# Kernel tuning notes

Measured on AMD Instinct MI355X. Metric: run time of the kernel, lower is better.

The kernel has to match this reference:

```python
import jax, jax.numpy as jnp
import numpy as np

N_HEADS = 8
D_EMBED = 512
D_HEAD = D_EMBED // N_HEADS


def setup_inputs() -> dict:
    key = jax.random.key(0)
    ks = jax.random.split(key, 5)
    x = jax.random.normal(ks[0], (1, 4096, D_EMBED), dtype=jnp.float32)
    # in_proj: Linear(d, 3d); out_proj: Linear(d, d). Stored as [in, out] for x @ W.
    scale_in = 1.0 / np.sqrt(D_EMBED)
    W_in = jax.random.uniform(ks[1], (D_EMBED, 3 * D_EMBED), jnp.float32, -scale_in, scale_in)
    b_in = jax.random.uniform(ks[2], (3 * D_EMBED,), jnp.float32, -scale_in, scale_in)
    W_out = jax.random.uniform(ks[3], (D_EMBED, D_EMBED), jnp.float32, -scale_in, scale_in)
    b_out = jax.random.uniform(ks[4], (D_EMBED,), jnp.float32, -scale_in, scale_in)
    return {"x": x, "W_in": W_in, "b_in": b_in, "W_out": W_out, "b_out": b_out,
            "causal_mask": 1}


def reference(x, W_in, b_in, W_out, b_out, causal_mask):
    B, S, D = x.shape
    qkv = x @ W_in + b_in                      # [B, S, 3D]
    q, k, v = jnp.split(qkv, 3, axis=-1)
    # [B, S, D] -> [B, H, S, d_head]
    def split_heads(t):
        return t.reshape(B, S, N_HEADS, D_HEAD).transpose(0, 2, 1, 3)
    q, k, v = split_heads(q), split_heads(k), split_heads(v)
    weight = jnp.einsum("bhqd,bhkd->bhqk", q, k)  # [B, H, S, S]
    if causal_mask:
        mask = jnp.triu(jnp.ones((S, S), dtype=bool), k=1)
        weight = jnp.where(mask, -jnp.inf, weight)
    weight = weight / jnp.sqrt(jnp.float32(D_HEAD)).astype(weight.dtype)
    weight = jax.nn.softmax(weight, axis=-1)
    out = jnp.einsum("bhqk,bhkd->bhqd", weight, v)  # [B, H, S, d_head]
    out = out.transpose(0, 2, 1, 3).reshape(B, S, D)
    return out @ W_out + b_out
```

## Files before the change

### kernel.cpp

```cpp
#include <hip/hip_runtime.h>
#include <math.h>

#define SEQ 4096
#define DM 512
#define NH 8
#define DH 64
#define TQK (3 * DM)
#define QSCALE 0.18033688011112042f

typedef __attribute__((ext_vector_type(8))) short bf16x8;
typedef __attribute__((ext_vector_type(4))) float floatx4;
typedef unsigned short ushort_t;

__device__ __forceinline__ floatx4 mfma16(bf16x8 a, bf16x8 b, floatx4 c) {
    return __builtin_amdgcn_mfma_f32_16x16x32_bf16(a, b, c, 0, 0, 0);
}
__device__ __forceinline__ float ex2(float x) { return __builtin_amdgcn_exp2f(x); }

__device__ __forceinline__ unsigned int pk2(float a, float b) {
    unsigned int ua = __float_as_uint(a); ua = (ua + 0x7FFFu + ((ua >> 16) & 1u)) >> 16;
    unsigned int ub = __float_as_uint(b); ub = (ub + 0x7FFFu + ((ub >> 16) & 1u)) >> 16;
    return ua | (ub << 16);
}
__device__ __forceinline__ unsigned short f2bf(float x) {
    unsigned int u = __float_as_uint(x);
    return (unsigned short)((u + 0x7FFFu + ((u >> 16) & 1u)) >> 16);
}
__device__ __forceinline__ float bflo(unsigned int u) { return __uint_as_float(u << 16); }
__device__ __forceinline__ float bfhi(unsigned int u) { return __uint_as_float(u & 0xFFFF0000u); }

__device__ __forceinline__ void gload_lds16(const void* g, void* l) {
    __builtin_amdgcn_global_load_lds(
        (const __attribute__((address_space(1))) unsigned int*)g,
        (__attribute__((address_space(3))) unsigned int*)l, 16, 0, 0);
}

#define DPPMAX(x, ctrl) \
    (x) = fmaxf((x), __int_as_float(__builtin_amdgcn_update_dpp(0, __float_as_int(x), (ctrl), 0xF, 0xF, true)))
__device__ __forceinline__ float row_max16(float x) {
    DPPMAX(x, 0xB1);
    DPPMAX(x, 0x4E);
    DPPMAX(x, 0x141);
    DPPMAX(x, 0x140);
    return x;
}

__global__ __launch_bounds__(256) void prep(const float* __restrict__ x,
                                            const float* __restrict__ W_in,
                                            const float* __restrict__ W_out,
                                            ushort_t* __restrict__ xb,
                                            ushort_t* __restrict__ wti,
                                            ushort_t* __restrict__ wto) {
    __shared__ float T[64][65];
    const int bid = blockIdx.x, tid = threadIdx.x;
    if (bid < 1024) {
        const int i = bid * 256 + tid;
        const float4* p = (const float4*)x + (size_t)i * 2;
        float4 f0 = p[0], f1 = p[1];
        ((uint4*)xb)[i] = make_uint4(pk2(f0.x, f0.y), pk2(f0.z, f0.w),
                                     pk2(f1.x, f1.y), pk2(f1.z, f1.w));
        return;
    }
    const float* W; ushort_t* WT; int N, K, n0, k0; bool qscale;
    if (bid < 1216) { int id = bid - 1024; W = W_in;  WT = wti; N = TQK; K = DM;
                      n0 = (id % 24) * 64; k0 = (id / 24) * 64; qscale = true; }
    else            { int id = bid - 1216; W = W_out; WT = wto; N = DM;  K = DM;
                      n0 = (id % 8) * 64;  k0 = (id / 8) * 64;  qscale = false; }
    {
        const int r = tid >> 2, g = tid & 3;
        const float* src = W + (size_t)(k0 + r) * N + n0 + g * 16;
#pragma unroll
        for (int i = 0; i < 4; i++) {
            float4 f = ((const float4*)src)[i];
            T[g * 16 + i * 4 + 0][r] = f.x;
            T[g * 16 + i * 4 + 1][r] = f.y;
            T[g * 16 + i * 4 + 2][r] = f.z;
            T[g * 16 + i * 4 + 3][r] = f.w;
        }
    }
    __syncthreads();
    const int nr = tid >> 2, g2 = tid & 3;
    const float sc = (qscale && (n0 + nr < DM)) ? QSCALE : 1.0f;
    unsigned int pk[8];
#pragma unroll
    for (int j = 0; j < 8; j++)
        pk[j] = pk2(T[nr][g2 * 16 + 2 * j] * sc, T[nr][g2 * 16 + 2 * j + 1] * sc);
    ushort_t* dst = WT + (size_t)(n0 + nr) * K + k0 + g2 * 16;
    ((uint4*)dst)[0] = make_uint4(pk[0], pk[1], pk[2], pk[3]);
    ((uint4*)dst)[1] = make_uint4(pk[4], pk[5], pk[6], pk[7]);
}

__global__ __launch_bounds__(256) void gemm_in(const ushort_t* __restrict__ A,
                                               const ushort_t* __restrict__ BT,
                                               const float* __restrict__ bias,
                                               ushort_t* __restrict__ Cv,
                                               ushort_t* __restrict__ vt_out) {
    __shared__ __align__(16) ushort_t As[2][128 * 64];
    __shared__ __align__(16) ushort_t Bs[2][128 * 64];
    const int tid  = threadIdx.x;
    const int lane = tid & 63;
    const int w    = tid >> 6;
    const int quad = lane >> 4;
    const int ln   = lane & 15;
    const int row0 = blockIdx.y * 128;
    const int col0 = blockIdx.x * 128;
    const int wm = w >> 1, wn = w & 1;
    const int srow = lane >> 3;
    const int js   = (lane & 7) ^ srow;
    const int K = DM, N = TQK;

    floatx4 acc[4][4];
#pragma unroll
    for (int i = 0; i < 4; i++)
#pragma unroll
        for (int j = 0; j < 4; j++) acc[i][j] = (floatx4){0.f, 0.f, 0.f, 0.f};

#pragma unroll
    for (int i = 0; i < 4; i++) {
        const int c = w * 4 + i;
        gload_lds16(A  + (size_t)(row0 + c * 8 + srow) * K + js * 8, &As[0][c * 512]);
        gload_lds16(BT + (size_t)(col0 + c * 8 + srow) * K + js * 8, &Bs[0][c * 512]);
    }

    for (int kt = 0; kt < 8; kt++) {
        const int cur = kt & 1;
        __syncthreads();
        if (kt < 7) {
            const int k0n = (kt + 1) << 6;
#pragma unroll
            for (int i = 0; i < 4; i++) {
                const int c = w * 4 + i;
                gload_lds16(A  + (size_t)(row0 + c * 8 + srow) * K + k0n + js * 8, &As[cur ^ 1][c * 512]);
                gload_lds16(BT + (size_t)(col0 + c * 8 + srow) * K + k0n + js * 8, &Bs[cur ^ 1][c * 512]);
            }
        }
#pragma unroll
        for (int s = 0; s < 2; s++) {
            bf16x8 af[4], bfr[4];
#pragma unroll
            for (int i = 0; i < 4; i++) {
                const int lm = wm * 64 + i * 16 + ln;
                af[i] = *(const bf16x8*)&As[cur][lm * 64 + ((s * 4 + quad) ^ (ln & 7)) * 8];
                const int lnn = wn * 64 + i * 16 + ln;
                bfr[i] = *(const bf16x8*)&Bs[cur][lnn * 64 + ((s * 4 + quad) ^ (ln & 7)) * 8];
            }
#pragma unroll
            for (int i = 0; i < 4; i++)
#pragma unroll
                for (int j = 0; j < 4; j++)
                    acc[i][j] = mfma16(af[i], bfr[j], acc[i][j]);
        }
    }

    if (col0 >= 2 * DM) {
#pragma unroll
        for (int j = 0; j < 4; j++) {
            const int n = col0 + wn * 64 + j * 16 + ln;
            const float bv = bias[n];
#pragma unroll
            for (int i = 0; i < 4; i++) {
                const int mb = row0 + wm * 64 + i * 16 + quad * 4;
                uint2 pkd;
                pkd.x = pk2(acc[i][j][0] + bv, acc[i][j][1] + bv);
                pkd.y = pk2(acc[i][j][2] + bv, acc[i][j][3] + bv);
                *(uint2*)&vt_out[(size_t)(n - 2 * DM) * SEQ + mb] = pkd;
            }
        }
        return;
    }

#pragma unroll
    for (int j = 0; j < 4; j++) {
        const int n = col0 + wn * 64 + j * 16 + ln;
        const float bv = bias[n] * ((n < DM) ? QSCALE : 1.0f);
#pragma unroll
        for (int i = 0; i < 4; i++) {
            const int mb = row0 + wm * 64 + i * 16 + quad * 4;
#pragma unroll
            for (int r = 0; r < 4; r++)
                Cv[(size_t)(mb + r) * N + n] = f2bf(acc[i][j][r] + bv);
        }
    }
}

__global__ __launch_bounds__(512) void attn_split(const ushort_t* __restrict__ qkv_b,
                                                  const ushort_t* __restrict__ vt,
                                                  ushort_t* __restrict__ po,
                                                  float2* __restrict__ pml) {
    __shared__ __align__(16) ushort_t Ks[2][64 * 64];
    __shared__ __align__(16) ushort_t Vs[2][64 * 64];
    __shared__ __align__(16) ushort_t Ps[128 * 72];

    const int tid  = threadIdx.x;
    const int lane = tid & 63;
    const int w    = tid >> 6;
    const int quad = lane >> 4;
    const int ln   = lane & 15;
    const int h    = blockIdx.y;

    const int e = 143 - (int)blockIdx.x;
    int g = 0;
    while (e >= 2 * (g + 1) * (g + 2)) g++;
    const int off = e - 2 * g * (g + 1);
    const int nc  = g + 1;
    const int qt  = 4 * g + off / nc;
    const int c   = off % nc;
    const int T   = 2 * qt + 2;
    const int jt0 = (c * T) / nc;
    const int jt1 = ((c + 1) * T) / nc;
    const int q0  = qt * 128;

    const ushort_t* qrow = qkv_b + (size_t)(q0 + w * 16 + ln) * TQK + h * DH;
    const bf16x8 a0 = *(const bf16x8*)(qrow + quad * 8);
    const bf16x8 a1 = *(const bf16x8*)(qrow + quad * 8 + 32);

    const short oneb = (short)0x3F80;
    const bf16x8 vone = {oneb, oneb, oneb, oneb, oneb, oneb, oneb, oneb};

    float m_q = -INFINITY;
    floatx4 o[4], ol;
#pragma unroll
    for (int t = 0; t < 4; t++) o[t] = (floatx4){0.f, 0.f, 0.f, 0.f};
    ol = (floatx4){0.f, 0.f, 0.f, 0.f};

    const int srow = lane >> 3;
    const int js   = (lane & 7) ^ srow;

    {
        const int k0 = jt0 * 64;
        gload_lds16(qkv_b + (size_t)(k0 + w * 8 + srow) * TQK + DM + h * DH + js * 8,
                    &Ks[0][w * 512]);
        gload_lds16(vt + (size_t)(h * DH + w * 8 + srow) * SEQ + k0 + js * 8,
                    &Vs[0][w * 512]);
    }

    for (int jt = jt0; jt < jt1; ++jt) {
        const int cur = (jt - jt0) & 1;
        const int k0  = jt * 64;
        __syncthreads();
        if (jt + 1 < jt1) {
            const int k0n = (jt + 1) * 64;
            gload_lds16(qkv_b + (size_t)(k0n + w * 8 + srow) * TQK + DM + h * DH + js * 8,
                        &Ks[cur ^ 1][w * 512]);
            gload_lds16(vt + (size_t)(h * DH + w * 8 + srow) * SEQ + k0n + js * 8,
                        &Vs[cur ^ 1][w * 512]);
        }

        floatx4 sa[4];
#pragma unroll
        for (int t = 0; t < 4; t++) {
            const int n = t * 16 + ln;
            const bf16x8 b0 = *(const bf16x8*)&Ks[cur][n * 64 + ((quad) ^ (ln & 7)) * 8];
            const bf16x8 b1 = *(const bf16x8*)&Ks[cur][n * 64 + ((4 + quad) ^ (ln & 7)) * 8];
            floatx4 acc = {0.f, 0.f, 0.f, 0.f};
            acc = mfma16(a0, b0, acc);
            acc = mfma16(a1, b1, acc);
            sa[t] = acc;
        }

        if (k0 + 63 > q0 + w * 16) {
#pragma unroll
            for (int t = 0; t < 4; t++) {
                const int cg2 = k0 + t * 16 + ln;
#pragma unroll
                for (int r = 0; r < 4; r++) {
                    const int rg = q0 + w * 16 + quad * 4 + r;
                    if (cg2 > rg) sa[t][r] = -INFINITY;
                }
            }
        }

        float mx = sa[0][0];
#pragma unroll
        for (int t = 0; t < 4; t++)
#pragma unroll
            for (int r = 0; r < 4; r++) mx = fmaxf(mx, sa[t][r]);
        mx = row_max16(mx);
        const float mn = fmaxf(fmaxf(m_q, mx), -1e30f);
        const float alpha = ex2(m_q - mn);
        m_q = mn;
#pragma unroll
        for (int t = 0; t < 4; t++)
#pragma unroll
            for (int r = 0; r < 4; r++) {
                const float p = ex2(sa[t][r] - mn);
                Ps[(w * 16 + quad * 4 + r) * 72 + t * 16 + ln] =
                    (ushort_t)(__float_as_uint(p) >> 16);
            }
        if (alpha < 1.0f) {
#pragma unroll
            for (int t = 0; t < 4; t++)
#pragma unroll
                for (int r = 0; r < 4; r++) o[t][r] *= alpha;
#pragma unroll
            for (int r = 0; r < 4; r++) ol[r] *= alpha;
        }

        __builtin_amdgcn_wave_barrier();

        const bf16x8 p0 = *(const bf16x8*)&Ps[(w * 16 + ln) * 72 + quad * 8];
        const bf16x8 p1 = *(const bf16x8*)&Ps[(w * 16 + ln) * 72 + quad * 8 + 32];
#pragma unroll
        for (int t = 0; t < 4; t++) {
            const int d = t * 16 + ln;
            const bf16x8 v0 = *(const bf16x8*)&Vs[cur][d * 64 + ((quad) ^ (ln & 7)) * 8];
            const bf16x8 v1 = *(const bf16x8*)&Vs[cur][d * 64 + ((4 + quad) ^ (ln & 7)) * 8];
            o[t] = mfma16(p0, v0, o[t]);
            o[t] = mfma16(p1, v1, o[t]);
        }
        ol = mfma16(p0, vone, ol);
        ol = mfma16(p1, vone, ol);
    }

    const size_t pbase  = ((size_t)h * 144 + e) * (128 * 64);
    const size_t mlbase = ((size_t)h * 144 + e) * 128;
#pragma unroll
    for (int t = 0; t < 4; t++)
#pragma unroll
        for (int r = 0; r < 4; r++)
            po[pbase + (size_t)(w * 16 + quad * 4 + r) * 64 + t * 16 + ln] = f2bf(o[t][r]);
    if (ln == 0) {
#pragma unroll
        for (int r = 0; r < 4; r++)
            pml[mlbase + w * 16 + quad * 4 + r] = make_float2(m_q, ol[r]);
    }
}

__global__ __launch_bounds__(512) void attn_combine(const ushort_t* __restrict__ po,
                                                    const float2* __restrict__ pml,
                                                    ushort_t* __restrict__ aob) {
    const int qt = blockIdx.x, h = blockIdx.y;
    const int gq = qt >> 2;
    const int nc = gq + 1;
    const int sbase = 2 * gq * (gq + 1) + (qt & 3) * nc;
    const int row = threadIdx.x >> 2, g = threadIdx.x & 3;

    float2 ml[8];
    float M = -INFINITY;
    for (int ci = 0; ci < nc; ci++) {
        ml[ci] = pml[((size_t)h * 144 + sbase + ci) * 128 + row];
        M = fmaxf(M, ml[ci].x);
    }
    float L = 0.f;
    float acc[16];
#pragma unroll
    for (int j = 0; j < 16; j++) acc[j] = 0.f;

    for (int ci = 0; ci < nc; ci++) {
        const float wgt = ex2(ml[ci].x - M);
        L += wgt * ml[ci].y;
        const ushort_t* p = po + ((size_t)h * 144 + sbase + ci) * (128 * 64)
                               + (size_t)row * 64 + g * 16;
        uint4 u0 = ((const uint4*)p)[0];
        uint4 u1 = ((const uint4*)p)[1];
        const unsigned int uu[8] = {u0.x, u0.y, u0.z, u0.w, u1.x, u1.y, u1.z, u1.w};
#pragma unroll
        for (int j = 0; j < 8; j++) {
            acc[2 * j]     += wgt * bflo(uu[j]);
            acc[2 * j + 1] += wgt * bfhi(uu[j]);
        }
    }
    const float inv = 1.0f / L;
    unsigned int pk[8];
#pragma unroll
    for (int j = 0; j < 8; j++)
        pk[j] = pk2(acc[2 * j] * inv, acc[2 * j + 1] * inv);
    ushort_t* dst = aob + (size_t)(qt * 128 + row) * DM + h * DH + g * 16;
    ((uint4*)dst)[0] = make_uint4(pk[0], pk[1], pk[2], pk[3]);
    ((uint4*)dst)[1] = make_uint4(pk[4], pk[5], pk[6], pk[7]);
}

__global__ __launch_bounds__(256) void gemm_out(const ushort_t* __restrict__ A,
                                                const ushort_t* __restrict__ BT,
                                                const float* __restrict__ bias,
                                                float* __restrict__ out) {
    __shared__ __align__(16) ushort_t As[2][128 * 64];
    __shared__ __align__(16) ushort_t Bs[2][64 * 64];
    const int tid  = threadIdx.x;
    const int lane = tid & 63;
    const int w    = tid >> 6;
    const int quad = lane >> 4;
    const int ln   = lane & 15;
    const int row0 = blockIdx.y * 128;
    const int col0 = blockIdx.x * 64;
    const int wm = w >> 1, wn = w & 1;
    const int srow = lane >> 3;
    const int js   = (lane & 7) ^ srow;

    floatx4 acc[4][2];
#pragma unroll
    for (int i = 0; i < 4; i++)
#pragma unroll
        for (int j = 0; j < 2; j++) acc[i][j] = (floatx4){0.f, 0.f, 0.f, 0.f};

#pragma unroll
    for (int i = 0; i < 4; i++) {
        const int c = w * 4 + i;
        gload_lds16(A + (size_t)(row0 + c * 8 + srow) * DM + js * 8, &As[0][c * 512]);
    }
#pragma unroll
    for (int i = 0; i < 2; i++) {
        const int c = w * 2 + i;
        gload_lds16(BT + (size_t)(col0 + c * 8 + srow) * DM + js * 8, &Bs[0][c * 512]);
    }

    for (int kt = 0; kt < 8; kt++) {
        const int cur = kt & 1;
        __syncthreads();
        if (kt < 7) {
            const int k0n = (kt + 1) << 6;
#pragma unroll
            for (int i = 0; i < 4; i++) {
                const int c = w * 4 + i;
                gload_lds16(A + (size_t)(row0 + c * 8 + srow) * DM + k0n + js * 8, &As[cur ^ 1][c * 512]);
            }
#pragma unroll
            for (int i = 0; i < 2; i++) {
                const int c = w * 2 + i;
                gload_lds16(BT + (size_t)(col0 + c * 8 + srow) * DM + k0n + js * 8, &Bs[cur ^ 1][c * 512]);
            }
        }
#pragma unroll
        for (int s = 0; s < 2; s++) {
            bf16x8 af[4], bfr[2];
#pragma unroll
            for (int i = 0; i < 4; i++) {
                const int lm = wm * 64 + i * 16 + ln;
                af[i] = *(const bf16x8*)&As[cur][lm * 64 + ((s * 4 + quad) ^ (ln & 7)) * 8];
            }
#pragma unroll
            for (int j = 0; j < 2; j++) {
                const int lnn = wn * 32 + j * 16 + ln;
                bfr[j] = *(const bf16x8*)&Bs[cur][lnn * 64 + ((s * 4 + quad) ^ (ln & 7)) * 8];
            }
#pragma unroll
            for (int i = 0; i < 4; i++)
#pragma unroll
                for (int j = 0; j < 2; j++)
                    acc[i][j] = mfma16(af[i], bfr[j], acc[i][j]);
        }
    }

#pragma unroll
    for (int j = 0; j < 2; j++) {
        const int n = col0 + wn * 32 + j * 16 + ln;
        const float bv = bias[n];
#pragma unroll
        for (int i = 0; i < 4; i++) {
            const int mb = row0 + wm * 64 + i * 16 + quad * 4;
#pragma unroll
            for (int r = 0; r < 4; r++)
                out[(size_t)(mb + r) * DM + n] = acc[i][j][r] + bv;
        }
    }
}

extern "C" void kernel_launch(void* const* d_in, const int* in_sizes, int n_in,
                              void* d_out, int out_size, void* d_ws, size_t ws_size,
                              hipStream_t stream) {
    const float* x     = (const float*)d_in[0];
    const float* W_in  = (const float*)d_in[1];
    const float* b_in  = (const float*)d_in[2];
    const float* W_out = (const float*)d_in[3];
    const float* b_out = (const float*)d_in[4];
    float* out = (float*)d_out;

    char* ws = (char*)d_ws;
    ushort_t* xb    = (ushort_t*)ws;
    ushort_t* wti   = (ushort_t*)(ws + (4u  << 20));
    ushort_t* wto   = (ushort_t*)(ws + (6u  << 20));
    ushort_t* qkv_b = (ushort_t*)(ws + (7u  << 20));
    ushort_t* vtb   = (ushort_t*)(ws + (19u << 20));
    ushort_t* po    = (ushort_t*)(ws + (23u << 20));
    float2*   pml   = (float2*)  (ws + (42u << 20));
    ushort_t* aob   = (ushort_t*)(ws + (44u << 20));

    prep<<<1280, 256, 0, stream>>>(x, W_in, W_out, xb, wti, wto);

    gemm_in<<<dim3(TQK / 128, SEQ / 128), 256, 0, stream>>>(xb, wti, b_in, qkv_b, vtb);

    attn_split<<<dim3(144, NH), 512, 0, stream>>>(qkv_b, vtb, po, pml);

    attn_combine<<<dim3(SEQ / 128, NH), 512, 0, stream>>>(po, pml, aob);

    gemm_out<<<dim3(DM / 64, SEQ / 128), 256, 0, stream>>>(aob, wto, b_out, out);
}
```

Measured before the change: 156.0 us.

## Restructure attention split kernel to keep P in registers with transposed S

The attention split kernel now computes S transposed (K as A operand), so each lane's exp'd probabilities can be packed straight into bf16 operands for a 16x16x16 MFMA against V. This removes the P round-trip through shared memory and the extra ones-vector MFMAs that tracked the row sum, which is now accumulated with cross-lane shuffles instead. Blocks shrink to 256 threads, with each wave handling two 16-row query groups so loaded K/V fragments are reused twice, and the work-tile ordering is recomputed with a loop. The trade-offs are more register pressure, truncating rather than rounding P and the output to bf16, and a split ordering that must stay consistent with the combine kernel.

```diff
diff --git a/kernel.cpp b/kernel.cpp
--- a/kernel.cpp
+++ b/kernel.cpp
@@ -9,11 +9,15 @@
 #define QSCALE 0.18033688011112042f
 
 typedef __attribute__((ext_vector_type(8))) short bf16x8;
+typedef __attribute__((ext_vector_type(4))) short short4v;
 typedef __attribute__((ext_vector_type(4))) float floatx4;
 typedef unsigned short ushort_t;
 
 __device__ __forceinline__ floatx4 mfma16(bf16x8 a, bf16x8 b, floatx4 c) {
     return __builtin_amdgcn_mfma_f32_16x16x32_bf16(a, b, c, 0, 0, 0);
+}
+__device__ __forceinline__ floatx4 mfma16k16(short4v a, short4v b, floatx4 c) {
+    return __builtin_amdgcn_mfma_f32_16x16x16bf16_1k(a, b, c, 0, 0, 0);
 }
 __device__ __forceinline__ float ex2(float x) { return __builtin_amdgcn_exp2f(x); }
 
@@ -26,23 +30,19 @@
     unsigned int u = __float_as_uint(x);
     return (unsigned short)((u + 0x7FFFu + ((u >> 16) & 1u)) >> 16);
 }
+__device__ __forceinline__ unsigned int pkt(float a, float b) {
+    return __builtin_amdgcn_perm(__float_as_uint(b), __float_as_uint(a), 0x07060302u);
+}
 __device__ __forceinline__ float bflo(unsigned int u) { return __uint_as_float(u << 16); }
 __device__ __forceinline__ float bfhi(unsigned int u) { return __uint_as_float(u & 0xFFFF0000u); }
+__device__ __forceinline__ short4v mk4(unsigned int lo, unsigned int hi) {
+    union { unsigned int u[2]; short4v v; } x; x.u[0] = lo; x.u[1] = hi; return x.v;
+}
 
 __device__ __forceinline__ void gload_lds16(const void* g, void* l) {
     __builtin_amdgcn_global_load_lds(
         (const __attribute__((address_space(1))) unsigned int*)g,
         (__attribute__((address_space(3))) unsigned int*)l, 16, 0, 0);
-}
-
-#define DPPMAX(x, ctrl) \
-    (x) = fmaxf((x), __int_as_float(__builtin_amdgcn_update_dpp(0, __float_as_int(x), (ctrl), 0xF, 0xF, true)))
-__device__ __forceinline__ float row_max16(float x) {
-    DPPMAX(x, 0xB1);
-    DPPMAX(x, 0x4E);
-    DPPMAX(x, 0x141);
-    DPPMAX(x, 0x140);
-    return x;
 }
 
 __global__ __launch_bounds__(256) void prep(const float* __restrict__ x,
@@ -183,13 +183,12 @@
     }
 }
 
-__global__ __launch_bounds__(512) void attn_split(const ushort_t* __restrict__ qkv_b,
-                                                  const ushort_t* __restrict__ vt,
-                                                  ushort_t* __restrict__ po,
-                                                  float2* __restrict__ pml) {
+__global__ __launch_bounds__(256, 3) void attn_split(const ushort_t* __restrict__ qkv_b,
+                                                     const ushort_t* __restrict__ vt,
+                                                     ushort_t* __restrict__ po,
+                                                     float2* __restrict__ pml) {
     __shared__ __align__(16) ushort_t Ks[2][64 * 64];
     __shared__ __align__(16) ushort_t Vs[2][64 * 64];
-    __shared__ __align__(16) ushort_t Ps[128 * 72];
 
     const int tid  = threadIdx.x;
     const int lane = tid & 63;
@@ -197,41 +196,51 @@
     const int quad = lane >> 4;
     const int ln   = lane & 15;
     const int h    = blockIdx.y;
-
-    const int e = 143 - (int)blockIdx.x;
-    int g = 0;
-    while (e >= 2 * (g + 1) * (g + 2)) g++;
-    const int off = e - 2 * g * (g + 1);
-    const int nc  = g + 1;
-    const int qt  = 4 * g + off / nc;
-    const int c   = off % nc;
+    const int lnx7 = ln & 7;
+    const int qh   = quad >> 1, ql = quad & 1;
+
+    int qt = 0, nc = 1, cc = 0;
+    {
+        int bx = blockIdx.x, acc = 0;
+        for (int q = 31; q >= 0; --q) {
+            const int n = (q >> 2) + 1;
+            if (bx < acc + n) { qt = q; nc = n; cc = bx - acc; break; }
+            acc += n;
+        }
+    }
     const int T   = 2 * qt + 2;
-    const int jt0 = (c * T) / nc;
-    const int jt1 = ((c + 1) * T) / nc;
+    const int jt0 = (cc * T) / nc;
+    const int jt1 = ((cc + 1) * T) / nc;
     const int q0  = qt * 128;
 
-    const ushort_t* qrow = qkv_b + (size_t)(q0 + w * 16 + ln) * TQK + h * DH;
-    const bf16x8 a0 = *(const bf16x8*)(qrow + quad * 8);
-    const bf16x8 a1 = *(const bf16x8*)(qrow + quad * 8 + 32);
-
-    const short oneb = (short)0x3F80;
-    const bf16x8 vone = {oneb, oneb, oneb, oneb, oneb, oneb, oneb, oneb};
-
-    float m_q = -INFINITY;
-    floatx4 o[4], ol;
-#pragma unroll
-    for (int t = 0; t < 4; t++) o[t] = (floatx4){0.f, 0.f, 0.f, 0.f};
-    ol = (floatx4){0.f, 0.f, 0.f, 0.f};
+    bf16x8 qb[2][2];
+#pragma unroll
+    for (int qg = 0; qg < 2; qg++) {
+        const ushort_t* qr = qkv_b + (size_t)(q0 + w * 32 + qg * 16 + ln) * TQK + h * DH;
+        qb[qg][0] = *(const bf16x8*)(qr + quad * 8);
+        qb[qg][1] = *(const bf16x8*)(qr + quad * 8 + 32);
+    }
+
+    float m_[2] = {-INFINITY, -INFINITY}, l_[2] = {0.f, 0.f};
+    floatx4 o[2][4];
+#pragma unroll
+    for (int qg = 0; qg < 2; qg++)
+#pragma unroll
+        for (int dt = 0; dt < 4; dt++) o[qg][dt] = (floatx4){0.f, 0.f, 0.f, 0.f};
 
     const int srow = lane >> 3;
     const int js   = (lane & 7) ^ srow;
 
     {
         const int k0 = jt0 * 64;
-        gload_lds16(qkv_b + (size_t)(k0 + w * 8 + srow) * TQK + DM + h * DH + js * 8,
-                    &Ks[0][w * 512]);
-        gload_lds16(vt + (size_t)(h * DH + w * 8 + srow) * SEQ + k0 + js * 8,
-                    &Vs[0][w * 512]);
+#pragma unroll
+        for (int i = 0; i < 2; i++) {
+            const int cg = w * 2 + i;
+            gload_lds16(qkv_b + (size_t)(k0 + cg * 8 + srow) * TQK + DM + h * DH + js * 8,
+                        &Ks[0][cg * 512]);
+            gload_lds16(vt + (size_t)(h * DH + cg * 8 + srow) * SEQ + k0 + js * 8,
+                        &Vs[0][cg * 512]);
+        }
     }
 
     for (int jt = jt0; jt < jt1; ++jt) {
@@ -240,89 +249,111 @@
         __syncthreads();
         if (jt + 1 < jt1) {
             const int k0n = (jt + 1) * 64;
-            gload_lds16(qkv_b + (size_t)(k0n + w * 8 + srow) * TQK + DM + h * DH + js * 8,
-                        &Ks[cur ^ 1][w * 512]);
-            gload_lds16(vt + (size_t)(h * DH + w * 8 + srow) * SEQ + k0n + js * 8,
-                        &Vs[cur ^ 1][w * 512]);
-        }
-
-        floatx4 sa[4];
+#pragma unroll
+            for (int i = 0; i < 2; i++) {
+                const int cg = w * 2 + i;
+                gload_lds16(qkv_b + (size_t)(k0n + cg * 8 + srow) * TQK + DM + h * DH + js * 8,
+                            &Ks[cur ^ 1][cg * 512]);
+                gload_lds16(vt + (size_t)(h * DH + cg * 8 + srow) * SEQ + k0n + js * 8,
+                            &Vs[cur ^ 1][cg * 512]);
+            }
+        }
+
+        bf16x8 kf[4][2];
 #pragma unroll
         for (int t = 0; t < 4; t++) {
-            const int n = t * 16 + ln;
-            const bf16x8 b0 = *(const bf16x8*)&Ks[cur][n * 64 + ((quad) ^ (ln & 7)) * 8];
-            const bf16x8 b1 = *(const bf16x8*)&Ks[cur][n * 64 + ((4 + quad) ^ (ln & 7)) * 8];
-            floatx4 acc = {0.f, 0.f, 0.f, 0.f};
-            acc = mfma16(a0, b0, acc);
-            acc = mfma16(a1, b1, acc);
-            sa[t] = acc;
-        }
-
-        if (k0 + 63 > q0 + w * 16) {
+            kf[t][0] = *(const bf16x8*)&Ks[cur][(t * 16 + ln) * 64 + ((quad) ^ lnx7) * 8];
+            kf[t][1] = *(const bf16x8*)&Ks[cur][(t * 16 + ln) * 64 + ((4 + quad) ^ lnx7) * 8];
+        }
+        short4v vf[4][4];
+#pragma unroll
+        for (int t = 0; t < 4; t++)
+#pragma unroll
+            for (int dt = 0; dt < 4; dt++)
+                vf[t][dt] = *(const short4v*)&Vs[cur][(dt * 16 + ln) * 64 +
+                                                     (((2 * t + qh) ^ lnx7) << 3) + (ql << 2)];
+
+#pragma unroll
+        for (int qg = 0; qg < 2; qg++) {
+            const int q = q0 + w * 32 + qg * 16 + ln;
+
+            floatx4 sa[4];
 #pragma unroll
             for (int t = 0; t < 4; t++) {
-                const int cg2 = k0 + t * 16 + ln;
+                floatx4 a = (floatx4){0.f, 0.f, 0.f, 0.f};
+                a = mfma16(kf[t][0], qb[qg][0], a);
+                a = mfma16(kf[t][1], qb[qg][1], a);
+                sa[t] = a;
+            }
+
+            if (k0 + 63 > q0 + w * 32 + qg * 16) {
+#pragma unroll
+                for (int t = 0; t < 4; t++)
+#pragma unroll
+                    for (int r = 0; r < 4; r++) {
+                        const int key = k0 + t * 16 + quad * 4 + r;
+                        if (key > q) sa[t][r] = -INFINITY;
+                    }
+            }
+
+            float mx = sa[0][0];
+#pragma unroll
+            for (int t = 0; t < 4; t++)
+#pragma unroll
+                for (int r = 0; r < 4; r++) mx = fmaxf(mx, sa[t][r]);
+            mx = fmaxf(mx, __shfl_xor(mx, 16));
+            mx = fmaxf(mx, __shfl_xor(mx, 32));
+            const float mn = fmaxf(fmaxf(m_[qg], mx), -1e30f);
+            const float alpha = ex2(m_[qg] - mn);
+            m_[qg] = mn;
+
+            float p[4][4];
+            float ls = 0.f;
+#pragma unroll
+            for (int t = 0; t < 4; t++)
 #pragma unroll
                 for (int r = 0; r < 4; r++) {
-                    const int rg = q0 + w * 16 + quad * 4 + r;
-                    if (cg2 > rg) sa[t][r] = -INFINITY;
+                    p[t][r] = ex2(sa[t][r] - mn);
+                    ls += p[t][r];
                 }
-            }
-        }
-
-        float mx = sa[0][0];
-#pragma unroll
-        for (int t = 0; t < 4; t++)
-#pragma unroll
-            for (int r = 0; r < 4; r++) mx = fmaxf(mx, sa[t][r]);
-        mx = row_max16(mx);
-        const float mn = fmaxf(fmaxf(m_q, mx), -1e30f);
-        const float alpha = ex2(m_q - mn);
-        m_q = mn;
-#pragma unroll
-        for (int t = 0; t < 4; t++)
-#pragma unroll
-            for (int r = 0; r < 4; r++) {
-                const float p = ex2(sa[t][r] - mn);
-                Ps[(w * 16 + quad * 4 + r) * 72 + t * 16 + ln] =
-                    (ushort_t)(__float_as_uint(p) >> 16);
-            }
-        if (alpha < 1.0f) {
+            ls += __shfl_xor(ls, 16);
+            ls += __shfl_xor(ls, 32);
+            l_[qg] = l_[qg] * alpha + ls;
+
+            float a4[4];
+#pragma unroll
+            for (int r = 0; r < 4; r++)
+                a4[r] = __shfl(alpha, (lane & 48) | (quad * 4 + r));
+#pragma unroll
+            for (int dt = 0; dt < 4; dt++)
+#pragma unroll
+                for (int r = 0; r < 4; r++) o[qg][dt][r] *= a4[r];
+
+            short4v pf[4];
 #pragma unroll
             for (int t = 0; t < 4; t++)
-#pragma unroll
-                for (int r = 0; r < 4; r++) o[t][r] *= alpha;
-#pragma unroll
-            for (int r = 0; r < 4; r++) ol[r] *= alpha;
-        }
-
-        __builtin_amdgcn_wave_barrier();
-
-        const bf16x8 p0 = *(const bf16x8*)&Ps[(w * 16 + ln) * 72 + quad * 8];
-        const bf16x8 p1 = *(const bf16x8*)&Ps[(w * 16 + ln) * 72 + quad * 8 + 32];
-#pragma unroll
-        for (int t = 0; t < 4; t++) {
-            const int d = t * 16 + ln;
-            const bf16x8 v0 = *(const bf16x8*)&Vs[cur][d * 64 + ((quad) ^ (ln & 7)) * 8];
-            const bf16x8 v1 = *(const bf16x8*)&Vs[cur][d * 64 + ((4 + quad) ^ (ln & 7)) * 8];
-            o[t] = mfma16(p0, v0, o[t]);
-            o[t] = mfma16(p1, v1, o[t]);
-        }
-        ol = mfma16(p0, vone, ol);
-        ol = mfma16(p1, vone, ol);
-    }
-
-    const size_t pbase  = ((size_t)h * 144 + e) * (128 * 64);
-    const size_t mlbase = ((size_t)h * 144 + e) * 128;
-#pragma unroll
-    for (int t = 0; t < 4; t++)
-#pragma unroll
-        for (int r = 0; r < 4; r++)
-            po[pbase + (size_t)(w * 16 + quad * 4 + r) * 64 + t * 16 + ln] = f2bf(o[t][r]);
-    if (ln == 0) {
-#pragma unroll
-        for (int r = 0; r < 4; r++)
-            pml[mlbase + w * 16 + quad * 4 + r] = make_float2(m_q, ol[r]);
+                pf[t] = mk4(pkt(p[t][0], p[t][1]), pkt(p[t][2], p[t][3]));
+
+#pragma unroll
+            for (int dt = 0; dt < 4; dt++)
+#pragma unroll
+                for (int t = 0; t < 4; t++)
+                    o[qg][dt] = mfma16k16(pf[t], vf[t][dt], o[qg][dt]);
+        }
+    }
+
+    const size_t pbase  = ((size_t)h * 144 + blockIdx.x) * (128 * 64);
+    const size_t mlbase = ((size_t)h * 144 + blockIdx.x) * 128;
+#pragma unroll
+    for (int qg = 0; qg < 2; qg++) {
+#pragma unroll
+        for (int dt = 0; dt < 4; dt++)
+#pragma unroll
+            for (int r = 0; r < 4; r++)
+                po[pbase + (size_t)(w * 32 + qg * 16 + quad * 4 + r) * 64 + dt * 16 + ln] =
+                    (ushort_t)(__float_as_uint(o[qg][dt][r]) >> 16);
+        if (quad == 0)
+            pml[mlbase + w * 32 + qg * 16 + ln] = make_float2(m_[qg], l_[qg]);
     }
 }
 
@@ -330,9 +361,9 @@
                                                     const float2* __restrict__ pml,
                                                     ushort_t* __restrict__ aob) {
     const int qt = blockIdx.x, h = blockIdx.y;
-    const int gq = qt >> 2;
-    const int nc = gq + 1;
-    const int sbase = 2 * gq * (gq + 1) + (qt & 3) * nc;
+    const int nc = (qt >> 2) + 1;
+    int sbase = 0;
+    for (int q = 31; q > qt; --q) sbase += (q >> 2) + 1;
     const int row = threadIdx.x >> 2, g = threadIdx.x & 3;
 
     float2 ml[8];
@@ -479,7 +510,7 @@
 
     gemm_in<<<dim3(TQK / 128, SEQ / 128), 256, 0, stream>>>(xb, wti, b_in, qkv_b, vtb);
 
-    attn_split<<<dim3(144, NH), 512, 0, stream>>>(qkv_b, vtb, po, pml);
+    attn_split<<<dim3(144, NH), 256, 0, stream>>>(qkv_b, vtb, po, pml);
 
     attn_combine<<<dim3(SEQ / 128, NH), 512, 0, stream>>>(po, pml, aob);
 
```

Measured after the change: 192.8 us. +23.6%, slower.

## Process two query row groups per wave in attention split kernel

Applied to the files above, without the earlier changes.

The attention split kernel now runs 4 waves of 256 threads instead of 8, and each wave handles 32 query rows as two 16-row groups. K fragments are loaded from LDS once and reused for both groups, and V fragments are likewise shared across the two P·V products. This halves LDS fragment reads per MFMA and the block synchronization cost. In exchange each wave holds more registers, and with launch bounds (256,3) there are fewer waves in flight to hide latency.

```diff
diff --git a/kernel.cpp b/kernel.cpp
--- a/kernel.cpp
+++ b/kernel.cpp
@@ -183,10 +183,10 @@
     }
 }
 
-__global__ __launch_bounds__(512) void attn_split(const ushort_t* __restrict__ qkv_b,
-                                                  const ushort_t* __restrict__ vt,
-                                                  ushort_t* __restrict__ po,
-                                                  float2* __restrict__ pml) {
+__global__ __launch_bounds__(256, 3) void attn_split(const ushort_t* __restrict__ qkv_b,
+                                                     const ushort_t* __restrict__ vt,
+                                                     ushort_t* __restrict__ po,
+                                                     float2* __restrict__ pml) {
     __shared__ __align__(16) ushort_t Ks[2][64 * 64];
     __shared__ __align__(16) ushort_t Vs[2][64 * 64];
     __shared__ __align__(16) ushort_t Ps[128 * 72];
@@ -197,6 +197,7 @@
     const int quad = lane >> 4;
     const int ln   = lane & 15;
     const int h    = blockIdx.y;
+    const int lnx7 = ln & 7;
 
     const int e = 143 - (int)blockIdx.x;
     int g = 0;
@@ -210,28 +211,39 @@
     const int jt1 = ((c + 1) * T) / nc;
     const int q0  = qt * 128;
 
-    const ushort_t* qrow = qkv_b + (size_t)(q0 + w * 16 + ln) * TQK + h * DH;
-    const bf16x8 a0 = *(const bf16x8*)(qrow + quad * 8);
-    const bf16x8 a1 = *(const bf16x8*)(qrow + quad * 8 + 32);
+    bf16x8 a0[2], a1[2];
+#pragma unroll
+    for (int qg = 0; qg < 2; qg++) {
+        const ushort_t* qrow = qkv_b + (size_t)(q0 + w * 32 + qg * 16 + ln) * TQK + h * DH;
+        a0[qg] = *(const bf16x8*)(qrow + quad * 8);
+        a1[qg] = *(const bf16x8*)(qrow + quad * 8 + 32);
+    }
 
     const short oneb = (short)0x3F80;
     const bf16x8 vone = {oneb, oneb, oneb, oneb, oneb, oneb, oneb, oneb};
 
-    float m_q = -INFINITY;
-    floatx4 o[4], ol;
-#pragma unroll
-    for (int t = 0; t < 4; t++) o[t] = (floatx4){0.f, 0.f, 0.f, 0.f};
-    ol = (floatx4){0.f, 0.f, 0.f, 0.f};
+    float m_q[2] = {-INFINITY, -INFINITY};
+    floatx4 o[2][4], ol[2];
+#pragma unroll
+    for (int qg = 0; qg < 2; qg++) {
+#pragma unroll
+        for (int t = 0; t < 4; t++) o[qg][t] = (floatx4){0.f, 0.f, 0.f, 0.f};
+        ol[qg] = (floatx4){0.f, 0.f, 0.f, 0.f};
+    }
 
     const int srow = lane >> 3;
     const int js   = (lane & 7) ^ srow;
 
     {
         const int k0 = jt0 * 64;
-        gload_lds16(qkv_b + (size_t)(k0 + w * 8 + srow) * TQK + DM + h * DH + js * 8,
-                    &Ks[0][w * 512]);
-        gload_lds16(vt + (size_t)(h * DH + w * 8 + srow) * SEQ + k0 + js * 8,
-                    &Vs[0][w * 512]);
+#pragma unroll
+        for (int i = 0; i < 2; i++) {
+            const int cg = w * 2 + i;
+            gload_lds16(qkv_b + (size_t)(k0 + cg * 8 + srow) * TQK + DM + h * DH + js * 8,
+                        &Ks[0][cg * 512]);
+            gload_lds16(vt + (size_t)(h * DH + cg * 8 + srow) * SEQ + k0 + js * 8,
+                        &Vs[0][cg * 512]);
+        }
     }
 
     for (int jt = jt0; jt < jt1; ++jt) {
@@ -240,89 +252,110 @@
         __syncthreads();
         if (jt + 1 < jt1) {
             const int k0n = (jt + 1) * 64;
-            gload_lds16(qkv_b + (size_t)(k0n + w * 8 + srow) * TQK + DM + h * DH + js * 8,
-                        &Ks[cur ^ 1][w * 512]);
-            gload_lds16(vt + (size_t)(h * DH + w * 8 + srow) * SEQ + k0n + js * 8,
-                        &Vs[cur ^ 1][w * 512]);
-        }
-
-        floatx4 sa[4];
+#pragma unroll
+            for (int i = 0; i < 2; i++) {
+                const int cg = w * 2 + i;
+                gload_lds16(qkv_b + (size_t)(k0n + cg * 8 + srow) * TQK + DM + h * DH + js * 8,
+                            &Ks[cur ^ 1][cg * 512]);
+                gload_lds16(vt + (size_t)(h * DH + cg * 8 + srow) * SEQ + k0n + js * 8,
+                            &Vs[cur ^ 1][cg * 512]);
+            }
+        }
+
+        bf16x8 kb0[4], kb1[4];
 #pragma unroll
         for (int t = 0; t < 4; t++) {
             const int n = t * 16 + ln;
-            const bf16x8 b0 = *(const bf16x8*)&Ks[cur][n * 64 + ((quad) ^ (ln & 7)) * 8];
-            const bf16x8 b1 = *(const bf16x8*)&Ks[cur][n * 64 + ((4 + quad) ^ (ln & 7)) * 8];
-            floatx4 acc = {0.f, 0.f, 0.f, 0.f};
-            acc = mfma16(a0, b0, acc);
-            acc = mfma16(a1, b1, acc);
-            sa[t] = acc;
-        }
-
-        if (k0 + 63 > q0 + w * 16) {
+            kb0[t] = *(const bf16x8*)&Ks[cur][n * 64 + ((quad) ^ lnx7) * 8];
+            kb1[t] = *(const bf16x8*)&Ks[cur][n * 64 + ((4 + quad) ^ lnx7) * 8];
+        }
+
+#pragma unroll
+        for (int qg = 0; qg < 2; qg++) {
+            floatx4 sa[4];
 #pragma unroll
             for (int t = 0; t < 4; t++) {
-                const int cg2 = k0 + t * 16 + ln;
+                floatx4 acc = {0.f, 0.f, 0.f, 0.f};
+                acc = mfma16(a0[qg], kb0[t], acc);
+                acc = mfma16(a1[qg], kb1[t], acc);
+                sa[t] = acc;
+            }
+
+            if (k0 + 63 > q0 + w * 32 + qg * 16) {
+#pragma unroll
+                for (int t = 0; t < 4; t++) {
+                    const int cg2 = k0 + t * 16 + ln;
+#pragma unroll
+                    for (int r = 0; r < 4; r++) {
+                        const int rg = q0 + w * 32 + qg * 16 + quad * 4 + r;
+                        if (cg2 > rg) sa[t][r] = -INFINITY;
+                    }
+                }
+            }
+
+            float mx = sa[0][0];
+#pragma unroll
+            for (int t = 0; t < 4; t++)
+#pragma unroll
+                for (int r = 0; r < 4; r++) mx = fmaxf(mx, sa[t][r]);
+            mx = row_max16(mx);
+            const float mn = fmaxf(fmaxf(m_q[qg], mx), -1e30f);
+            const float alpha = ex2(m_q[qg] - mn);
+            m_q[qg] = mn;
+#pragma unroll
+            for (int t = 0; t < 4; t++)
 #pragma unroll
                 for (int r = 0; r < 4; r++) {
-                    const int rg = q0 + w * 16 + quad * 4 + r;
-                    if (cg2 > rg) sa[t][r] = -INFINITY;
+                    const float p = ex2(sa[t][r] - mn);
+                    Ps[(w * 32 + qg * 16 + quad * 4 + r) * 72 + t * 16 + ln] =
+                        (ushort_t)(__float_as_uint(p) >> 16);
                 }
-            }
-        }
-
-        float mx = sa[0][0];
-#pragma unroll
-        for (int t = 0; t < 4; t++)
-#pragma unroll
-            for (int r = 0; r < 4; r++) mx = fmaxf(mx, sa[t][r]);
-        mx = row_max16(mx);
-        const float mn = fmaxf(fmaxf(m_q, mx), -1e30f);
-        const float alpha = ex2(m_q - mn);
-        m_q = mn;
-#pragma unroll
-        for (int t = 0; t < 4; t++)
-#pragma unroll
-            for (int r = 0; r < 4; r++) {
-                const float p = ex2(sa[t][r] - mn);
-                Ps[(w * 16 + quad * 4 + r) * 72 + t * 16 + ln] =
-                    (ushort_t)(__float_as_uint(p) >> 16);
-            }
-        if (alpha < 1.0f) {
-#pragma unroll
-            for (int t = 0; t < 4; t++)
-#pragma unroll
-                for (int r = 0; r < 4; r++) o[t][r] *= alpha;
-#pragma unroll
-            for (int r = 0; r < 4; r++) ol[r] *= alpha;
+            if (alpha < 1.0f) {
+#pragma unroll
+                for (int t = 0; t < 4; t++)
+#pragma unroll
+                    for (int r = 0; r < 4; r++) o[qg][t][r] *= alpha;
+#pragma unroll
+                for (int r = 0; r < 4; r++) ol[qg][r] *= alpha;
+            }
         }
 
         __builtin_amdgcn_wave_barrier();
 
-        const bf16x8 p0 = *(const bf16x8*)&Ps[(w * 16 + ln) * 72 + quad * 8];
-        const bf16x8 p1 = *(const bf16x8*)&Ps[(w * 16 + ln) * 72 + quad * 8 + 32];
 #pragma unroll
         for (int t = 0; t < 4; t++) {
             const int d = t * 16 + ln;
-            const bf16x8 v0 = *(const bf16x8*)&Vs[cur][d * 64 + ((quad) ^ (ln & 7)) * 8];
-            const bf16x8 v1 = *(const bf16x8*)&Vs[cur][d * 64 + ((4 + quad) ^ (ln & 7)) * 8];
-            o[t] = mfma16(p0, v0, o[t]);
-            o[t] = mfma16(p1, v1, o[t]);
-        }
-        ol = mfma16(p0, vone, ol);
-        ol = mfma16(p1, vone, ol);
+            const bf16x8 v0 = *(const bf16x8*)&Vs[cur][d * 64 + ((quad) ^ lnx7) * 8];
+            const bf16x8 v1 = *(const bf16x8*)&Vs[cur][d * 64 + ((4 + quad) ^ lnx7) * 8];
+#pragma unroll
+            for (int qg = 0; qg < 2; qg++) {
+                const bf16x8 p0 = *(const bf16x8*)&Ps[(w * 32 + qg * 16 + ln) * 72 + quad * 8];
+                const bf16x8 p1 = *(const bf16x8*)&Ps[(w * 32 + qg * 16 + ln) * 72 + quad * 8 + 32];
+                o[qg][t] = mfma16(p0, v0, o[qg][t]);
+                o[qg][t] = mfma16(p1, v1, o[qg][t]);
+                if (t == 0) {
+                    ol[qg] = mfma16(p0, vone, ol[qg]);
+                    ol[qg] = mfma16(p1, vone, ol[qg]);
+                }
+            }
+        }
     }
 
     const size_t pbase  = ((size_t)h * 144 + e) * (128 * 64);
     const size_t mlbase = ((size_t)h * 144 + e) * 128;
 #pragma unroll
-    for (int t = 0; t < 4; t++)
-#pragma unroll
-        for (int r = 0; r < 4; r++)
-            po[pbase + (size_t)(w * 16 + quad * 4 + r) * 64 + t * 16 + ln] = f2bf(o[t][r]);
-    if (ln == 0) {
-#pragma unroll
-        for (int r = 0; r < 4; r++)
-            pml[mlbase + w * 16 + quad * 4 + r] = make_float2(m_q, ol[r]);
+    for (int qg = 0; qg < 2; qg++) {
+#pragma unroll
+        for (int t = 0; t < 4; t++)
+#pragma unroll
+            for (int r = 0; r < 4; r++)
+                po[pbase + (size_t)(w * 32 + qg * 16 + quad * 4 + r) * 64 + t * 16 + ln] =
+                    f2bf(o[qg][t][r]);
+        if (ln == 0) {
+#pragma unroll
+            for (int r = 0; r < 4; r++)
+                pml[mlbase + w * 32 + qg * 16 + quad * 4 + r] = make_float2(m_q[qg], ol[qg][r]);
+        }
     }
 }
 
@@ -479,7 +512,7 @@
 
     gemm_in<<<dim3(TQK / 128, SEQ / 128), 256, 0, stream>>>(xb, wti, b_in, qkv_b, vtb);
 
-    attn_split<<<dim3(144, NH), 512, 0, stream>>>(qkv_b, vtb, po, pml);
+    attn_split<<<dim3(144, NH), 256, 0, stream>>>(qkv_b, vtb, po, pml);
 
     attn_combine<<<dim3(SEQ / 128, NH), 512, 0, stream>>>(po, pml, aob);
 
```

New measurement: 156.0 us. Within noise of the previous version (+0.0%).
